# Kernel tuning notes

Measured on AMD Instinct MI355X. Metric: run time of the kernel, lower is better.

Reference implementation:

```python
import jax, jax.numpy as jnp
import numpy as np

T, N, G2, R, E, I, O = 20, 512, 16, 128, 64, 2, 5


def setup_inputs() -> dict:
    key = jax.random.key(0)
    ks = jax.random.split(key, 12)
    s = 0.02
    return {
        "nodes": jax.random.normal(ks[0], (T, N, I), jnp.float32),
        "grids": jax.random.uniform(ks[1], (T, N, N, G2), jnp.float32),
        "hidden_states": jnp.zeros((N, R), jnp.float32),
        "cell_states": jnp.zeros((N, R), jnp.float32),
        "W_in": jax.random.normal(ks[2], (E, I), jnp.float32) * s,
        "b_in": jnp.zeros((E,), jnp.float32),
        "W_tensor": jax.random.normal(ks[3], (E, G2 * R), jnp.float32) * s,
        "b_tensor": jnp.zeros((E,), jnp.float32),
        "W_ih": jax.random.normal(ks[4], (4 * R, 2 * E), jnp.float32) * s,
        "b_ih": jnp.zeros((4 * R,), jnp.float32),
        "W_hh": jax.random.normal(ks[5], (4 * R, R), jnp.float32) * s,
        "b_hh": jnp.zeros((4 * R,), jnp.float32),
        "W_out": jax.random.normal(ks[6], (O, R), jnp.float32) * s,
        "b_out": jnp.zeros((O,), jnp.float32),
    }


def reference(nodes, grids, hidden_states, cell_states,
              W_in, b_in, W_tensor, b_tensor,
              W_ih, b_ih, W_hh, b_hh, W_out, b_out):
    def step(carry, xs):
        h, c = carry
        nodes_t, grid_t = xs  # [N,I], [N,N,G2]
        # social tensor: for each node, grid[node].T @ hidden -> [N, G2, R]
        social = jnp.einsum('nmg,mr->ngr', grid_t, h).reshape(N, G2 * R)
        ie = jax.nn.relu(nodes_t @ W_in.T + b_in)          # [N,E]
        te = jax.nn.relu(social @ W_tensor.T + b_tensor)   # [N,E]
        x = jnp.concatenate([ie, te], axis=1)              # [N,2E]
        gates = x @ W_ih.T + b_ih + h @ W_hh.T + b_hh      # [N,4R]
        i_g, f_g, g_g, o_g = jnp.split(gates, 4, axis=1)   # torch LSTMCell order
        c2 = jax.nn.sigmoid(f_g) * c + jax.nn.sigmoid(i_g) * jnp.tanh(g_g)
        h2 = jax.nn.sigmoid(o_g) * jnp.tanh(c2)
        out = h2 @ W_out.T + b_out                         # [N,O]
        return (h2, c2), out

    (h_f, c_f), outputs = jax.lax.scan(step, (hidden_states, cell_states), (nodes, grids))
    return outputs, h_f, c_f
```

## Files before the change

kernel.cpp:

```cpp
#include <hip/hip_runtime.h>

#define TT 20
#define NNODE 512
#define G2C 16
#define RCH 128
#define ECH 64
#define ICH 2
#define OCH 5
#define KSOC 8192
#define KSPLIT 16
#define KCH 512

#define OFF_H    0u
#define OFF_C    65536u
#define OFF_HT   131072u
#define OFF_PART 655360u
#define OFF_WGT  1179648u
#define OFF_WHT  1245184u
#define OFF_WTT  1310720u
#define OFF_BS   1441792u

__device__ __forceinline__ double sigd(double x){ return 1.0/(1.0+exp(-x)); }

__global__ void k_init(const float* __restrict__ h0, const float* __restrict__ c0,
                       const float* __restrict__ W_ih, const float* __restrict__ b_ih,
                       const float* __restrict__ W_hh, const float* __restrict__ b_hh,
                       const float* __restrict__ W_tensor, double* __restrict__ ws) {
  int tid = blockIdx.x*blockDim.x + threadIdx.x;
  int nthr = gridDim.x*blockDim.x;
  double* h = ws + OFF_H; double* c = ws + OFF_C;
  double* WgT = ws + OFF_WGT; double* WhT = ws + OFF_WHT;
  double* WtT = ws + OFF_WTT; double* bs = ws + OFF_BS;
  for (int i = tid; i < NNODE*RCH; i += nthr) { h[i] = (double)h0[i]; c[i] = (double)c0[i]; }
  for (int i = tid; i < 65536; i += nthr) {
    int q = i & 3; int pr = i >> 2; int r = pr & 127; int p = pr >> 7;
    WgT[i] = (double)W_ih[(q*128 + r)*128 + p];
    WhT[i] = (double)W_hh[(q*128 + r)*128 + p];
  }
  for (int i = tid; i < 131072; i += nthr) {
    int e = i & 63; int q2 = i >> 6;
    WtT[i] = (double)W_tensor[e*2048 + q2];
  }
  for (int i = tid; i < 512; i += nthr) {
    int q = i & 3; int r = i >> 2;
    bs[i] = (double)b_ih[q*128 + r] + (double)b_hh[q*128 + r];
  }
}

__global__ __launch_bounds__(256) void k_ht(double* __restrict__ ws) {
  __shared__ double hb[2][128];
  const double* __restrict__ h = ws + OFF_H;
  const double* __restrict__ WtT = ws + OFF_WTT;
  double* __restrict__ Ht = ws + OFF_HT;
  const int m0 = blockIdx.x << 1;
  const int tid = threadIdx.x;
  hb[tid>>7][tid&127] = h[(size_t)(m0 + (tid>>7))*RCH + (tid&127)];
  __syncthreads();
  const int e = tid & 63, gq = tid >> 6;
  double acc[2][4] = {};
  for (int rr = 0; rr < 128; ++rr) {
    double hv0 = hb[0][rr], hv1 = hb[1][rr];
    #pragma unroll
    for (int jg = 0; jg < 4; ++jg) {
      double wv = WtT[((size_t)(((gq<<2)+jg)*RCH + rr))*ECH + e];
      acc[0][jg] += hv0*wv; acc[1][jg] += hv1*wv;
    }
  }
  #pragma unroll
  for (int n2 = 0; n2 < 2; ++n2)
    #pragma unroll
    for (int jg = 0; jg < 4; ++jg)
      Ht[(((size_t)(m0+n2))*G2C + (gq<<2)+jg)*ECH + e] = acc[n2][jg];
}

__global__ __launch_bounds__(256) void k_social(const float* __restrict__ grids,
                                                double* __restrict__ ws, int t) {
  __shared__ __align__(16) double sgd[16*260];
  float* sgf = (float*)sgd;
  const double* __restrict__ Ht = ws + OFF_HT;
  double* __restrict__ part = ws + OFF_PART;
  const int kc = blockIdx.x & (KSPLIT-1);
  const int n0 = (blockIdx.x >> 4) << 4;
  const int kb = kc * KCH;
  const int tid = threadIdx.x;
  const float* gbase = grids + (size_t)t*NNODE*KSOC;
  for (int i = tid; i < 16*128; i += 256) {
    int row = i >> 7; int c4 = i & 127;
    float4 v = *(const float4*)(gbase + (size_t)(n0+row)*KSOC + kb + (c4<<2));
    *(float4*)(&sgf[row*520 + (c4<<2)]) = v;
  }
  __syncthreads();
  const int lane = tid & 63;
  const int wv = tid >> 6;
  const int e0 = (lane & 15) << 2;
  const int nq = lane >> 4;
  double acc[4][4] = {};
  const int kl0 = wv << 7;
  const double* htp = Ht + (size_t)(kb + kl0)*ECH + e0;
  for (int kk = 0; kk < 128; ++kk) {
    double2 b01 = *(const double2*)(htp + (size_t)kk*ECH);
    double2 b23 = *(const double2*)(htp + (size_t)kk*ECH + 2);
    const int kl = kl0 + kk;
    #pragma unroll
    for (int jn = 0; jn < 4; ++jn) {
      double av = (double)sgf[((jn<<2)+nq)*520 + kl];
      acc[jn][0] += av*b01.x; acc[jn][1] += av*b01.y;
      acc[jn][2] += av*b23.x; acc[jn][3] += av*b23.y;
    }
  }
  __syncthreads();
  if (wv > 0) {
    double* rp = sgd + ((size_t)(wv-1)*64 + lane)*16;
    #pragma unroll
    for (int jn = 0; jn < 4; ++jn)
      #pragma unroll
      for (int je = 0; je < 4; ++je) rp[(jn<<2)+je] = acc[jn][je];
  }
  __syncthreads();
  if (wv == 0) {
    #pragma unroll
    for (int w = 0; w < 3; ++w) {
      const double* rp = sgd + ((size_t)w*64 + lane)*16;
      #pragma unroll
      for (int jn = 0; jn < 4; ++jn)
        #pragma unroll
        for (int je = 0; je < 4; ++je) acc[jn][je] += rp[(jn<<2)+je];
    }
    #pragma unroll
    for (int jn = 0; jn < 4; ++jn) {
      double* pp = part + ((size_t)kc*NNODE + n0 + (jn<<2) + nq)*ECH + e0;
      pp[0]=acc[jn][0]; pp[1]=acc[jn][1]; pp[2]=acc[jn][2]; pp[3]=acc[jn][3];
    }
  }
}

__global__ __launch_bounds__(256) void k_cell(const float* __restrict__ nodes,
    const float* __restrict__ W_in, const float* __restrict__ b_in,
    const float* __restrict__ b_tensor,
    const float* __restrict__ W_out, const float* __restrict__ b_out,
    double* __restrict__ ws, float* __restrict__ outp,
    float* __restrict__ hf, float* __restrict__ cf, int t) {
  __shared__ double xbuf[2][128];
  __shared__ double hbuf[2][128];
  __shared__ double h2buf[2][128];
  double* __restrict__ h = ws + OFF_H;
  double* __restrict__ c = ws + OFF_C;
  double* __restrict__ Ht = ws + OFF_HT;
  const double* __restrict__ part = ws + OFF_PART;
  const double* __restrict__ WgT = ws + OFF_WGT;
  const double* __restrict__ WhT = ws + OFF_WHT;
  const double* __restrict__ WtT = ws + OFF_WTT;
  const double* __restrict__ bs = ws + OFF_BS;
  const int tid = threadIdx.x;
  const int nl = tid >> 7, lane = tid & 127;
  const int m0 = blockIdx.x << 1;
  const int m = m0 + nl;
  hbuf[nl][lane] = h[(size_t)m*RCH + lane];
  if (lane < 64) {
    double teacc = (double)b_tensor[lane];
    for (int pc = 0; pc < KSPLIT; ++pc)
      teacc += part[((size_t)pc*NNODE + m)*ECH + lane];
    xbuf[nl][64+lane] = fmax(teacc, 0.0);
  } else {
    int e = lane - 64;
    double n0v = (double)nodes[((size_t)t*NNODE + m)*ICH + 0];
    double n1v = (double)nodes[((size_t)t*NNODE + m)*ICH + 1];
    double ie = n0v*(double)W_in[e*2] + n1v*(double)W_in[e*2+1] + (double)b_in[e];
    xbuf[nl][e] = fmax(ie, 0.0);
  }
  __syncthreads();
  const int r = lane;
  double a0=0, a1=0, a2=0, a3=0;
  const double* wgp = WgT + ((size_t)r << 2);
  const double* whp = WhT + ((size_t)r << 2);
  #pragma unroll 2
  for (int p = 0; p < 128; ++p) {
    double xv = xbuf[nl][p], hv = hbuf[nl][p];
    double2 g01 = *(const double2*)(wgp + ((size_t)p << 9));
    double2 g23 = *(const double2*)(wgp + ((size_t)p << 9) + 2);
    double2 q01 = *(const double2*)(whp + ((size_t)p << 9));
    double2 q23 = *(const double2*)(whp + ((size_t)p << 9) + 2);
    a0 += xv*g01.x + hv*q01.x;
    a1 += xv*g01.y + hv*q01.y;
    a2 += xv*g23.x + hv*q23.x;
    a3 += xv*g23.y + hv*q23.y;
  }
  double ig = sigd(a0 + bs[(r<<2)+0]);
  double fg = sigd(a1 + bs[(r<<2)+1]);
  double gg = tanh(a2 + bs[(r<<2)+2]);
  double og = sigd(a3 + bs[(r<<2)+3]);
  double cold = c[(size_t)m*RCH + r];
  double c2 = fg*cold + ig*gg;
  double h2 = og*tanh(c2);
  c[(size_t)m*RCH + r] = c2;
  h[(size_t)m*RCH + r] = h2;
  h2buf[nl][r] = h2;
  if (t == TT-1) {
    hf[(size_t)m*RCH + r] = (float)h2;
    cf[(size_t)m*RCH + r] = (float)c2;
  }
  __syncthreads();
  const int w = tid >> 6;
  if ((w & 1) == 0) {
    const int node = w >> 1, l = tid & 63;
    #pragma unroll
    for (int oo = 0; oo < OCH; ++oo) {
      double v = h2buf[node][l]*(double)W_out[oo*RCH + l]
               + h2buf[node][64+l]*(double)W_out[oo*RCH + 64 + l];
      for (int off = 32; off > 0; off >>= 1) v += __shfl_down(v, off, 64);
      if (l == 0)
        outp[((size_t)t*NNODE + m0 + node)*OCH + oo] = (float)(v + (double)b_out[oo]);
    }
  }
  if (t < TT-1) {
    const int e = tid & 63, gq = tid >> 6;
    double acc[2][4] = {};
    for (int rr = 0; rr < 128; ++rr) {
      double hv0 = h2buf[0][rr], hv1 = h2buf[1][rr];
      #pragma unroll
      for (int jg = 0; jg < 4; ++jg) {
        double wv = WtT[((size_t)(((gq<<2)+jg)*RCH + rr))*ECH + e];
        acc[0][jg] += hv0*wv; acc[1][jg] += hv1*wv;
      }
    }
    #pragma unroll
    for (int n2 = 0; n2 < 2; ++n2)
      #pragma unroll
      for (int jg = 0; jg < 4; ++jg)
        Ht[(((size_t)(m0+n2))*G2C + (gq<<2)+jg)*ECH + e] = acc[n2][jg];
  }
}

extern "C" void kernel_launch(void* const* d_in, const int* in_sizes, int n_in,
                              void* d_out, int out_size, void* d_ws, size_t ws_size,
                              hipStream_t stream) {
  const float* nodes    = (const float*)d_in[0];
  const float* grids    = (const float*)d_in[1];
  const float* h0       = (const float*)d_in[2];
  const float* c0       = (const float*)d_in[3];
  const float* W_in     = (const float*)d_in[4];
  const float* b_in     = (const float*)d_in[5];
  const float* W_tensor = (const float*)d_in[6];
  const float* b_tensor = (const float*)d_in[7];
  const float* W_ih     = (const float*)d_in[8];
  const float* b_ih     = (const float*)d_in[9];
  const float* W_hh     = (const float*)d_in[10];
  const float* b_hh     = (const float*)d_in[11];
  const float* W_out    = (const float*)d_in[12];
  const float* b_out    = (const float*)d_in[13];
  double* ws = (double*)d_ws;
  float* outp = (float*)d_out;
  float* hf = outp + (size_t)TT*NNODE*OCH;
  float* cf = hf + (size_t)NNODE*RCH;

  k_init<<<256, 256, 0, stream>>>(h0, c0, W_ih, b_ih, W_hh, b_hh, W_tensor, ws);
  k_ht<<<256, 256, 0, stream>>>(ws);
  for (int t = 0; t < TT; ++t) {
    k_social<<<512, 256, 0, stream>>>(grids, ws, t);
    k_cell<<<256, 256, 0, stream>>>(nodes, W_in, b_in, b_tensor, W_out, b_out,
                                    ws, outp, hf, cf, t);
  }
}
```

Baseline: 1.723 ms.

## Retile LSTM cell and split Ht/output projection into separate kernel

The LSTM cell kernel is rewritten so each block handles 16 nodes by 8 hidden units across all four gates, using a concatenated [W_ih|W_hh] weight layout. Each weight row is now reused across 16 nodes instead of 2. The hidden-to-tensor projection and the output projection move into a new k_ht_out kernel tiled over 16 nodes and 2 grid cells. k_social's inner loop is unrolled by two with float2 shared loads and a smaller padded stride. This adds a third launch per timestep and moves h through global memory between kernels.

```diff
diff --git a/kernel.cpp b/kernel.cpp
--- a/kernel.cpp
+++ b/kernel.cpp
@@ -10,13 +10,13 @@
 #define KSOC 8192
 #define KSPLIT 16
 #define KCH 512
+#define SGS 516
 
 #define OFF_H    0u
 #define OFF_C    65536u
 #define OFF_HT   131072u
 #define OFF_PART 655360u
-#define OFF_WGT  1179648u
-#define OFF_WHT  1245184u
+#define OFF_WCAT 1179648u
 #define OFF_WTT  1310720u
 #define OFF_BS   1441792u
 
@@ -29,53 +29,23 @@
   int tid = blockIdx.x*blockDim.x + threadIdx.x;
   int nthr = gridDim.x*blockDim.x;
   double* h = ws + OFF_H; double* c = ws + OFF_C;
-  double* WgT = ws + OFF_WGT; double* WhT = ws + OFF_WHT;
-  double* WtT = ws + OFF_WTT; double* bs = ws + OFF_BS;
+  double* Wcat = ws + OFF_WCAT; double* WtT = ws + OFF_WTT;
+  double* bs = ws + OFF_BS;
   for (int i = tid; i < NNODE*RCH; i += nthr) { h[i] = (double)h0[i]; c[i] = (double)c0[i]; }
-  for (int i = tid; i < 65536; i += nthr) {
-    int q = i & 3; int pr = i >> 2; int r = pr & 127; int p = pr >> 7;
-    WgT[i] = (double)W_ih[(q*128 + r)*128 + p];
-    WhT[i] = (double)W_hh[(q*128 + r)*128 + p];
-  }
-  for (int i = tid; i < 131072; i += nthr) {
+  for (int i = tid; i < 512*256; i += nthr) {
+    int kk = i & 255; int gc = i >> 8;
+    Wcat[i] = (kk < 128) ? (double)W_ih[gc*128 + kk] : (double)W_hh[gc*128 + (kk-128)];
+  }
+  for (int i = tid; i < 2048*64; i += nthr) {
     int e = i & 63; int q2 = i >> 6;
     WtT[i] = (double)W_tensor[e*2048 + q2];
   }
-  for (int i = tid; i < 512; i += nthr) {
-    int q = i & 3; int r = i >> 2;
-    bs[i] = (double)b_ih[q*128 + r] + (double)b_hh[q*128 + r];
-  }
-}
-
-__global__ __launch_bounds__(256) void k_ht(double* __restrict__ ws) {
-  __shared__ double hb[2][128];
-  const double* __restrict__ h = ws + OFF_H;
-  const double* __restrict__ WtT = ws + OFF_WTT;
-  double* __restrict__ Ht = ws + OFF_HT;
-  const int m0 = blockIdx.x << 1;
-  const int tid = threadIdx.x;
-  hb[tid>>7][tid&127] = h[(size_t)(m0 + (tid>>7))*RCH + (tid&127)];
-  __syncthreads();
-  const int e = tid & 63, gq = tid >> 6;
-  double acc[2][4] = {};
-  for (int rr = 0; rr < 128; ++rr) {
-    double hv0 = hb[0][rr], hv1 = hb[1][rr];
-    #pragma unroll
-    for (int jg = 0; jg < 4; ++jg) {
-      double wv = WtT[((size_t)(((gq<<2)+jg)*RCH + rr))*ECH + e];
-      acc[0][jg] += hv0*wv; acc[1][jg] += hv1*wv;
-    }
-  }
-  #pragma unroll
-  for (int n2 = 0; n2 < 2; ++n2)
-    #pragma unroll
-    for (int jg = 0; jg < 4; ++jg)
-      Ht[(((size_t)(m0+n2))*G2C + (gq<<2)+jg)*ECH + e] = acc[n2][jg];
+  for (int i = tid; i < 512; i += nthr) bs[i] = (double)b_ih[i] + (double)b_hh[i];
 }
 
 __global__ __launch_bounds__(256) void k_social(const float* __restrict__ grids,
                                                 double* __restrict__ ws, int t) {
-  __shared__ __align__(16) double sgd[16*260];
+  __shared__ __align__(16) double sgd[4160];
   float* sgf = (float*)sgd;
   const double* __restrict__ Ht = ws + OFF_HT;
   double* __restrict__ part = ws + OFF_PART;
@@ -87,7 +57,7 @@
   for (int i = tid; i < 16*128; i += 256) {
     int row = i >> 7; int c4 = i & 127;
     float4 v = *(const float4*)(gbase + (size_t)(n0+row)*KSOC + kb + (c4<<2));
-    *(float4*)(&sgf[row*520 + (c4<<2)]) = v;
+    *(float4*)(&sgf[row*SGS + (c4<<2)]) = v;
   }
   __syncthreads();
   const int lane = tid & 63;
@@ -97,15 +67,21 @@
   double acc[4][4] = {};
   const int kl0 = wv << 7;
   const double* htp = Ht + (size_t)(kb + kl0)*ECH + e0;
-  for (int kk = 0; kk < 128; ++kk) {
-    double2 b01 = *(const double2*)(htp + (size_t)kk*ECH);
-    double2 b23 = *(const double2*)(htp + (size_t)kk*ECH + 2);
+  #pragma unroll 2
+  for (int kk = 0; kk < 128; kk += 2) {
+    double2 b0a = *(const double2*)(htp + (size_t)kk*ECH);
+    double2 b0b = *(const double2*)(htp + (size_t)kk*ECH + 2);
+    double2 b1a = *(const double2*)(htp + (size_t)(kk+1)*ECH);
+    double2 b1b = *(const double2*)(htp + (size_t)(kk+1)*ECH + 2);
     const int kl = kl0 + kk;
     #pragma unroll
     for (int jn = 0; jn < 4; ++jn) {
-      double av = (double)sgf[((jn<<2)+nq)*520 + kl];
-      acc[jn][0] += av*b01.x; acc[jn][1] += av*b01.y;
-      acc[jn][2] += av*b23.x; acc[jn][3] += av*b23.y;
+      float2 av2 = *(const float2*)(&sgf[((jn<<2)+nq)*SGS + kl]);
+      double a0 = (double)av2.x, a1 = (double)av2.y;
+      acc[jn][0] += a0*b0a.x + a1*b1a.x;
+      acc[jn][1] += a0*b0a.y + a1*b1a.y;
+      acc[jn][2] += a0*b0b.x + a1*b1b.x;
+      acc[jn][3] += a0*b0b.y + a1*b1b.y;
     }
   }
   __syncthreads();
@@ -137,97 +113,129 @@
 __global__ __launch_bounds__(256) void k_cell(const float* __restrict__ nodes,
     const float* __restrict__ W_in, const float* __restrict__ b_in,
     const float* __restrict__ b_tensor,
-    const float* __restrict__ W_out, const float* __restrict__ b_out,
-    double* __restrict__ ws, float* __restrict__ outp,
-    float* __restrict__ hf, float* __restrict__ cf, int t) {
-  __shared__ double xbuf[2][128];
-  __shared__ double hbuf[2][128];
-  __shared__ double h2buf[2][128];
+    double* __restrict__ ws, float* __restrict__ hf, float* __restrict__ cf, int t) {
+  __shared__ double xh[16][258];
+  __shared__ double gbuf[32][17];
   double* __restrict__ h = ws + OFF_H;
   double* __restrict__ c = ws + OFF_C;
-  double* __restrict__ Ht = ws + OFF_HT;
   const double* __restrict__ part = ws + OFF_PART;
-  const double* __restrict__ WgT = ws + OFF_WGT;
-  const double* __restrict__ WhT = ws + OFF_WHT;
-  const double* __restrict__ WtT = ws + OFF_WTT;
+  const double* __restrict__ Wcat = ws + OFF_WCAT;
   const double* __restrict__ bs = ws + OFF_BS;
   const int tid = threadIdx.x;
-  const int nl = tid >> 7, lane = tid & 127;
-  const int m0 = blockIdx.x << 1;
-  const int m = m0 + nl;
-  hbuf[nl][lane] = h[(size_t)m*RCH + lane];
-  if (lane < 64) {
-    double teacc = (double)b_tensor[lane];
-    for (int pc = 0; pc < KSPLIT; ++pc)
-      teacc += part[((size_t)pc*NNODE + m)*ECH + lane];
-    xbuf[nl][64+lane] = fmax(teacc, 0.0);
-  } else {
-    int e = lane - 64;
-    double n0v = (double)nodes[((size_t)t*NNODE + m)*ICH + 0];
-    double n1v = (double)nodes[((size_t)t*NNODE + m)*ICH + 1];
-    double ie = n0v*(double)W_in[e*2] + n1v*(double)W_in[e*2+1] + (double)b_in[e];
-    xbuf[nl][e] = fmax(ie, 0.0);
-  }
-  __syncthreads();
-  const int r = lane;
-  double a0=0, a1=0, a2=0, a3=0;
-  const double* wgp = WgT + ((size_t)r << 2);
-  const double* whp = WhT + ((size_t)r << 2);
-  #pragma unroll 2
-  for (int p = 0; p < 128; ++p) {
-    double xv = xbuf[nl][p], hv = hbuf[nl][p];
-    double2 g01 = *(const double2*)(wgp + ((size_t)p << 9));
-    double2 g23 = *(const double2*)(wgp + ((size_t)p << 9) + 2);
-    double2 q01 = *(const double2*)(whp + ((size_t)p << 9));
-    double2 q23 = *(const double2*)(whp + ((size_t)p << 9) + 2);
-    a0 += xv*g01.x + hv*q01.x;
-    a1 += xv*g01.y + hv*q01.y;
-    a2 += xv*g23.x + hv*q23.x;
-    a3 += xv*g23.y + hv*q23.y;
-  }
-  double ig = sigd(a0 + bs[(r<<2)+0]);
-  double fg = sigd(a1 + bs[(r<<2)+1]);
-  double gg = tanh(a2 + bs[(r<<2)+2]);
-  double og = sigd(a3 + bs[(r<<2)+3]);
-  double cold = c[(size_t)m*RCH + r];
-  double c2 = fg*cold + ig*gg;
-  double h2 = og*tanh(c2);
-  c[(size_t)m*RCH + r] = c2;
-  h[(size_t)m*RCH + r] = h2;
-  h2buf[nl][r] = h2;
-  if (t == TT-1) {
-    hf[(size_t)m*RCH + r] = (float)h2;
-    cf[(size_t)m*RCH + r] = (float)c2;
-  }
-  __syncthreads();
-  const int w = tid >> 6;
-  if ((w & 1) == 0) {
-    const int node = w >> 1, l = tid & 63;
-    #pragma unroll
-    for (int oo = 0; oo < OCH; ++oo) {
-      double v = h2buf[node][l]*(double)W_out[oo*RCH + l]
-               + h2buf[node][64+l]*(double)W_out[oo*RCH + 64 + l];
-      for (int off = 32; off > 0; off >>= 1) v += __shfl_down(v, off, 64);
-      if (l == 0)
-        outp[((size_t)t*NNODE + m0 + node)*OCH + oo] = (float)(v + (double)b_out[oo]);
-    }
-  }
-  if (t < TT-1) {
-    const int e = tid & 63, gq = tid >> 6;
-    double acc[2][4] = {};
+  const int nc = blockIdx.x >> 4;
+  const int rc = blockIdx.x & 15;
+  const int m0 = nc << 4;
+  {
+    const int e = tid & 63;
+    #pragma unroll
+    for (int pass = 0; pass < 4; ++pass) {
+      const int n = (tid >> 6) + (pass << 2);
+      const int m = m0 + n;
+      double te = (double)b_tensor[e];
+      for (int kc = 0; kc < KSPLIT; ++kc)
+        te += part[((size_t)kc*NNODE + m)*ECH + e];
+      double n0v = (double)nodes[((size_t)t*NNODE + m)*ICH + 0];
+      double n1v = (double)nodes[((size_t)t*NNODE + m)*ICH + 1];
+      double ie = n0v*(double)W_in[e*2] + n1v*(double)W_in[e*2+1] + (double)b_in[e];
+      xh[n][e] = fmax(ie, 0.0);
+      xh[n][64+e] = fmax(te, 0.0);
+    }
+    const int r = tid & 127;
+    #pragma unroll
+    for (int pass = 0; pass < 8; ++pass) {
+      const int n = (tid >> 7) + (pass << 1);
+      xh[n][128+r] = h[(size_t)(m0+n)*RCH + r];
+    }
+  }
+  __syncthreads();
+  {
+    const int n = tid & 15, tg = tid >> 4;
+    const int q0 = tg >> 3, jr = tg & 7;
+    const int gc0 = q0*128 + rc*8 + jr;
+    const int gc1 = (q0+2)*128 + rc*8 + jr;
+    const double* w0 = Wcat + (size_t)gc0*256;
+    const double* w1 = Wcat + (size_t)gc1*256;
+    double a0 = 0.0, a1 = 0.0;
+    #pragma unroll 8
+    for (int kk = 0; kk < 256; kk += 2) {
+      double2 xv = *(const double2*)(&xh[n][kk]);
+      double2 wa = *(const double2*)(w0 + kk);
+      double2 wb = *(const double2*)(w1 + kk);
+      a0 += xv.x*wa.x + xv.y*wa.y;
+      a1 += xv.x*wb.x + xv.y*wb.y;
+    }
+    gbuf[tg][n]    = a0 + bs[gc0];
+    gbuf[tg+16][n] = a1 + bs[gc1];
+  }
+  __syncthreads();
+  if (tid < 128) {
+    const int n = tid >> 3, jr = tid & 7;
+    const int m = m0 + n, r = rc*8 + jr;
+    double ig = sigd(gbuf[jr][n]);
+    double fg = sigd(gbuf[8+jr][n]);
+    double gg = tanh(gbuf[16+jr][n]);
+    double og = sigd(gbuf[24+jr][n]);
+    double cold = c[(size_t)m*RCH + r];
+    double c2 = fg*cold + ig*gg;
+    double h2v = og*tanh(c2);
+    c[(size_t)m*RCH + r] = c2;
+    h[(size_t)m*RCH + r] = h2v;
+    if (t == TT-1) {
+      hf[(size_t)m*RCH + r] = (float)h2v;
+      cf[(size_t)m*RCH + r] = (float)c2;
+    }
+  }
+}
+
+__global__ __launch_bounds__(256) void k_ht_out(const float* __restrict__ W_out,
+    const float* __restrict__ b_out, double* __restrict__ ws,
+    float* __restrict__ outp, int t, int wout) {
+  __shared__ double h2b[16][130];
+  const double* __restrict__ h = ws + OFF_H;
+  const double* __restrict__ WtT = ws + OFF_WTT;
+  double* __restrict__ Ht = ws + OFF_HT;
+  const int tid = threadIdx.x;
+  const int mc = blockIdx.x >> 3;
+  const int gc2 = blockIdx.x & 7;
+  const int m0 = mc << 4, g0 = gc2 << 1;
+  {
+    const int r = tid & 127;
+    #pragma unroll
+    for (int pass = 0; pass < 8; ++pass) {
+      const int n = (tid >> 7) + (pass << 1);
+      h2b[n][r] = h[(size_t)(m0+n)*RCH + r];
+    }
+  }
+  __syncthreads();
+  {
+    const int e = tid & 63, mh = tid >> 6;
+    const double* wt0 = WtT + (size_t)(g0*128)*ECH + e;
+    const double* wt1 = WtT + (size_t)((g0+1)*128)*ECH + e;
+    double acc[4][2] = {};
+    #pragma unroll 4
     for (int rr = 0; rr < 128; ++rr) {
-      double hv0 = h2buf[0][rr], hv1 = h2buf[1][rr];
+      double w0 = wt0[(size_t)rr*ECH];
+      double w1 = wt1[(size_t)rr*ECH];
       #pragma unroll
-      for (int jg = 0; jg < 4; ++jg) {
-        double wv = WtT[((size_t)(((gq<<2)+jg)*RCH + rr))*ECH + e];
-        acc[0][jg] += hv0*wv; acc[1][jg] += hv1*wv;
+      for (int mi = 0; mi < 4; ++mi) {
+        double hv = h2b[(mh<<2)+mi][rr];
+        acc[mi][0] += hv*w0;
+        acc[mi][1] += hv*w1;
       }
     }
     #pragma unroll
-    for (int n2 = 0; n2 < 2; ++n2)
-      #pragma unroll
-      for (int jg = 0; jg < 4; ++jg)
-        Ht[(((size_t)(m0+n2))*G2C + (gq<<2)+jg)*ECH + e] = acc[n2][jg];
+    for (int mi = 0; mi < 4; ++mi) {
+      const int m = m0 + (mh<<2) + mi;
+      Ht[((size_t)m*G2C + g0    )*ECH + e] = acc[mi][0];
+      Ht[((size_t)m*G2C + g0 + 1)*ECH + e] = acc[mi][1];
+    }
+  }
+  if (gc2 == 0 && wout && tid < 80) {
+    const int mi = tid / OCH, oo = tid % OCH;
+    double v = (double)b_out[oo];
+    for (int r = 0; r < 128; ++r)
+      v += h2b[mi][r]*(double)W_out[oo*RCH + r];
+    outp[((size_t)t*NNODE + m0 + mi)*OCH + oo] = (float)v;
   }
 }
 
@@ -254,10 +262,10 @@
   float* cf = hf + (size_t)NNODE*RCH;
 
   k_init<<<256, 256, 0, stream>>>(h0, c0, W_ih, b_ih, W_hh, b_hh, W_tensor, ws);
-  k_ht<<<256, 256, 0, stream>>>(ws);
+  k_ht_out<<<256, 256, 0, stream>>>(W_out, b_out, ws, outp, 0, 0);
   for (int t = 0; t < TT; ++t) {
     k_social<<<512, 256, 0, stream>>>(grids, ws, t);
-    k_cell<<<256, 256, 0, stream>>>(nodes, W_in, b_in, b_tensor, W_out, b_out,
-                                    ws, outp, hf, cf, t);
-  }
-}
+    k_cell<<<512, 256, 0, stream>>>(nodes, W_in, b_in, b_tensor, ws, hf, cf, t);
+    k_ht_out<<<256, 256, 0, stream>>>(W_out, b_out, ws, outp, t, 1);
+  }
+}
```

After: 1.397 ms. 1.23x faster.
